# Kernel tuning notes

Measured on AMD Instinct MI355X. Metric: run time of the kernel, lower is better.

Reference implementation:

```python
import jax, jax.numpy as jnp
import numpy as np

NUM_HEADS = 4
EPS = 1e-5

def _proj(x, W, b):
    # 1x1x1 Conv3d == channel-wise linear: x [B,C,H,W,D], W [Cout,Cin], b [Cout]
    return jnp.einsum('oc,bchwd->bohwd', W, x) + b[None, :, None, None, None]

def setup_inputs() -> dict:
    key = jax.random.key(0)
    ks = jax.random.split(key, 12)
    B, C, H, W, D = 2, 128, 16, 16, 16
    s = 1.0 / np.sqrt(C)
    inp = {
        'query_features': jax.random.normal(ks[0], (B, C, H, W, D), jnp.float32),
        'key_value_features': jax.random.normal(ks[1], (B, C, H, W, D), jnp.float32),
        'Wq': jax.random.normal(ks[2], (C, C), jnp.float32) * s,
        'bq': jax.random.normal(ks[3], (C,), jnp.float32) * 0.01,
        'Wk': jax.random.normal(ks[4], (C, C), jnp.float32) * s,
        'bk': jax.random.normal(ks[5], (C,), jnp.float32) * 0.01,
        'Wv': jax.random.normal(ks[6], (C, C), jnp.float32) * s,
        'bv': jax.random.normal(ks[7], (C,), jnp.float32) * 0.01,
        'Wo': jax.random.normal(ks[8], (C, C), jnp.float32) * s,
        'bo': jax.random.normal(ks[9], (C,), jnp.float32) * 0.01,
    }
    return inp

def reference(query_features, key_value_features, Wq, bq, Wk, bk, Wv, bv, Wo, bo):
    B, C, H, W, D = query_features.shape
    hd = C // NUM_HEADS  # head_dim
    N = H * W * D
    Q = _proj(query_features, Wq, bq).reshape(B, NUM_HEADS, hd, N)
    K = _proj(key_value_features, Wk, bk).reshape(B, NUM_HEADS, hd, N)
    V = _proj(key_value_features, Wv, bv).reshape(B, NUM_HEADS, hd, N)
    scale = hd ** -0.5
    attn = jnp.einsum('bhdn,bhdm->bhnm', Q, K) * scale  # [B,h,N,N]
    attn = jax.nn.softmax(attn, axis=-1)
    out = jnp.einsum('bhnm,bhdm->bhdn', attn, V).reshape(B, C, H, W, D)
    out = _proj(out, Wo, bo)
    res = query_features + out
    # InstanceNorm3d (affine=False): normalize over spatial dims per (B,C)
    mu = jnp.mean(res, axis=(2, 3, 4), keepdims=True)
    var = jnp.var(res, axis=(2, 3, 4), keepdims=True)
    return (res - mu) * jax.lax.rsqrt(var + EPS)
```

## Files before the change

### kernel.cpp

```cpp
#include <hip/hip_runtime.h>
#include <hip/hip_bf16.h>

typedef unsigned short u16;
typedef unsigned int u32;
typedef __bf16 bf16_t;
typedef bf16_t bf16x8 __attribute__((ext_vector_type(8)));
typedef float f32x4 __attribute__((ext_vector_type(4)));

#define NTOT 4096
#define CCH 128

__device__ __forceinline__ float bf2f(u16 x) {
    return __uint_as_float(((u32)x) << 16);
}
__device__ __forceinline__ u32 pkbf(float a, float b) {
    __hip_bfloat162 h = __float22bfloat162_rn(make_float2(a, b));
    u32 r; __builtin_memcpy(&r, &h, 4); return r;
}
__device__ __forceinline__ u16 f2bf(float a) {
    return (u16)(pkbf(a, a) & 0xffffu);
}
union U4B8 { uint4 u4; u32 u[4]; bf16x8 v; };

__global__ __launch_bounds__(256) void proj_kernel(
    const float* __restrict__ xq, const float* __restrict__ xkv,
    const float* __restrict__ Wq, const float* __restrict__ bq_,
    const float* __restrict__ Wk, const float* __restrict__ bk_,
    const float* __restrict__ Wv, const float* __restrict__ bv_,
    u16* __restrict__ Qt, u16* __restrict__ Kt, u16* __restrict__ Vn)
{
    const int nt = blockIdx.x;
    const int ct = blockIdx.y;
    const int pb = blockIdx.z;
    const int p = pb >> 1, b = pb & 1;
    const float* X    = (p == 0) ? xq : xkv;
    const float* W    = (p == 0) ? Wq : (p == 1) ? Wk : Wv;
    const float* bias = (p == 0) ? bq_ : (p == 1) ? bk_ : bv_;
    const int n0 = nt * 64;
    const int tid = threadIdx.x;

    __shared__ u16 Xt[64 * 128];
    #pragma unroll
    for (int k = 0; k < 4; ++k) {
        int n = tid & 63;
        int c = (tid >> 6) + k * 4;
        float f[8];
        #pragma unroll
        for (int j = 0; j < 8; ++j)
            f[j] = X[((size_t)(b * CCH) + 8 * c + j) * NTOT + n0 + n];
        uint4 vv = {pkbf(f[0], f[1]), pkbf(f[2], f[3]), pkbf(f[4], f[5]), pkbf(f[6], f[7])};
        *(uint4*)(Xt + n * 128 + ((c ^ (n & 7)) * 8)) = vv;
    }
    __syncthreads();

    const int wave = tid >> 6, lane = tid & 63;
    const int quad = lane >> 4, l16 = lane & 15;
    f32x4 acc[2] = {{0.f, 0.f, 0.f, 0.f}, {0.f, 0.f, 0.f, 0.f}};

    #pragma unroll
    for (int kk = 0; kk < 4; ++kk) {
        bf16x8 bx = *(const bf16x8*)(Xt + (wave * 16 + l16) * 128 +
                                     (((kk * 4 + quad) ^ (l16 & 7)) * 8));
        #pragma unroll
        for (int hf = 0; hf < 2; ++hf) {
            const float* wrow = W + (size_t)(ct * 32 + hf * 16 + l16) * 128 + kk * 32 + quad * 8;
            float4 f0 = *(const float4*)(wrow);
            float4 f1 = *(const float4*)(wrow + 4);
            U4B8 aw;
            aw.u[0] = pkbf(f0.x, f0.y); aw.u[1] = pkbf(f0.z, f0.w);
            aw.u[2] = pkbf(f1.x, f1.y); aw.u[3] = pkbf(f1.z, f1.w);
            acc[hf] = __builtin_amdgcn_mfma_f32_16x16x32_bf16(aw.v, bx, acc[hf], 0, 0, 0);
        }
    }

    const float scl = (p == 0) ? 0.25503486703f : 1.0f;
    const int n = n0 + wave * 16 + l16;
    #pragma unroll
    for (int hf = 0; hf < 2; ++hf) {
        float4 b4 = *(const float4*)(bias + ct * 32 + hf * 16 + quad * 4);
        float v0 = (acc[hf][0] + b4.x) * scl;
        float v1 = (acc[hf][1] + b4.y) * scl;
        float v2 = (acc[hf][2] + b4.z) * scl;
        float v3 = (acc[hf][3] + b4.w) * scl;
        if (p < 2) {
            u16* dst = (p == 0 ? Qt : Kt) +
                ((size_t)(b * 4 + ct) * NTOT + n) * 32 + hf * 16 + quad * 4;
            uint2 vv = {pkbf(v0, v1), pkbf(v2, v3)};
            *(uint2*)dst = vv;
        } else {
            int c = ct * 32 + hf * 16 + quad * 4;
            u16* dst = Vn + (size_t)(b * CCH + c) * NTOT + n;
            dst[0 * NTOT] = f2bf(v0); dst[1 * NTOT] = f2bf(v1);
            dst[2 * NTOT] = f2bf(v2); dst[3 * NTOT] = f2bf(v3);
        }
    }
}

__global__ __launch_bounds__(256, 4) void flash_attn_kernel(
    const u16* __restrict__ Qt, const u16* __restrict__ Kt,
    const u16* __restrict__ Vn, u16* __restrict__ pO, float* __restrict__ pL)
{
    const int bh = blockIdx.z, kc = blockIdx.y;
    const int wave = threadIdx.x >> 6, lane = threadIdx.x & 63;
    const int q = lane >> 4, l16 = lane & 15;
    const int q0w = blockIdx.x * 128 + wave * 32;

    const u16* Qbh = Qt + (size_t)bh * NTOT * 32;
    const u16* Kbh = Kt + (size_t)bh * NTOT * 32;
    const u16* Vg  = Vn + ((size_t)((bh >> 2) * CCH + (bh & 3) * 32)) * NTOT;

    __shared__ u16 Kb[2][2048];
    __shared__ u16 Vb[2][2048];
    __shared__ u16 Pb[4][2048];

    const int kbase = kc * 1024;

    bf16x8 bq0 = *(const bf16x8*)(Qbh + (size_t)(q0w + l16) * 32 + q * 8);
    bf16x8 bq1 = *(const bf16x8*)(Qbh + (size_t)(q0w + 16 + l16) * 32 + q * 8);

    const size_t ksrc = (size_t)(wave * 16 + l16) * 32 + q * 8;
    const size_t vsrc = (size_t)((wave & 1) * 16 + l16) * NTOT + (wave >> 1) * 32 + q * 8;
    const int kv_dst = wave * 512 + lane * 8;

    uint4 kreg = *(const uint4*)(Kbh + (size_t)kbase * 32 + ksrc);
    uint4 vreg = *(const uint4*)(Vg + vsrc + kbase);
    *(uint4*)(&Kb[0][kv_dst]) = kreg;
    *(uint4*)(&Vb[0][kv_dst]) = vreg;
    __syncthreads();

    f32x4 o00 = {0,0,0,0}, o01 = {0,0,0,0};
    f32x4 o10 = {0,0,0,0}, o11 = {0,0,0,0};
    const f32x4 zero = {0,0,0,0};
    float lp0 = 0.f, lp1 = 0.f;

    u16* pw = &Pb[wave][0];
    const int pwr = (q >> 1) * 128 + l16 * 8 + (q & 1) * 4;

    for (int it = 0; it < 16; ++it) {
        const int cur = it & 1;
        if (it < 15) {
            const int m1 = kbase + (it + 1) * 64;
            kreg = *(const uint4*)(Kbh + (size_t)m1 * 32 + ksrc);
            vreg = *(const uint4*)(Vg + vsrc + m1);
        }
        f32x4 s0[4], s1[4];
        #pragma unroll
        for (int t = 0; t < 4; ++t) {
            bf16x8 ak = *(const bf16x8*)(&Kb[cur][t * 512 + lane * 8]);
            s0[t] = __builtin_amdgcn_mfma_f32_16x16x32_bf16(ak, bq0, zero, 0, 0, 0);
            s1[t] = __builtin_amdgcn_mfma_f32_16x16x32_bf16(ak, bq1, zero, 0, 0, 0);
        }
        #pragma unroll
        for (int t = 0; t < 4; ++t) {
            float p0 = __builtin_amdgcn_exp2f(s0[t][0]);
            float p1 = __builtin_amdgcn_exp2f(s0[t][1]);
            float p2 = __builtin_amdgcn_exp2f(s0[t][2]);
            float p3 = __builtin_amdgcn_exp2f(s0[t][3]);
            lp0 += (p0 + p1) + (p2 + p3);
            uint2 wv = {pkbf(p0, p1), pkbf(p2, p3)};
            *(uint2*)(pw + (t >> 1) * 512 + (t & 1) * 256 + pwr) = wv;
        }
        #pragma unroll
        for (int t = 0; t < 4; ++t) {
            float p0 = __builtin_amdgcn_exp2f(s1[t][0]);
            float p1 = __builtin_amdgcn_exp2f(s1[t][1]);
            float p2 = __builtin_amdgcn_exp2f(s1[t][2]);
            float p3 = __builtin_amdgcn_exp2f(s1[t][3]);
            lp1 += (p0 + p1) + (p2 + p3);
            uint2 wv = {pkbf(p0, p1), pkbf(p2, p3)};
            *(uint2*)(pw + 1024 + (t >> 1) * 512 + (t & 1) * 256 + pwr) = wv;
        }
        #pragma unroll
        for (int mc = 0; mc < 2; ++mc) {
            bf16x8 av0 = *(const bf16x8*)(&Vb[cur][(mc * 2 + 0) * 512 + lane * 8]);
            bf16x8 av1 = *(const bf16x8*)(&Vb[cur][(mc * 2 + 1) * 512 + lane * 8]);
            bf16x8 pb0 = *(const bf16x8*)(pw + mc * 512 + lane * 8);
            bf16x8 pb1 = *(const bf16x8*)(pw + 1024 + mc * 512 + lane * 8);
            o00 = __builtin_amdgcn_mfma_f32_16x16x32_bf16(av0, pb0, o00, 0, 0, 0);
            o01 = __builtin_amdgcn_mfma_f32_16x16x32_bf16(av1, pb0, o01, 0, 0, 0);
            o10 = __builtin_amdgcn_mfma_f32_16x16x32_bf16(av0, pb1, o10, 0, 0, 0);
            o11 = __builtin_amdgcn_mfma_f32_16x16x32_bf16(av1, pb1, o11, 0, 0, 0);
        }
        if (it < 15) {
            const int nb = (it + 1) & 1;
            *(uint4*)(&Kb[nb][kv_dst]) = kreg;
            *(uint4*)(&Vb[nb][kv_dst]) = vreg;
        }
        __syncthreads();
    }

    lp0 += __shfl_xor(lp0, 16); lp0 += __shfl_xor(lp0, 32);
    lp1 += __shfl_xor(lp1, 16); lp1 += __shfl_xor(lp1, 32);

    const size_t ob = ((size_t)(kc * 8 + bh) * NTOT + q0w + l16) * 32 + q * 4;
    uint2 w00 = {pkbf(o00[0], o00[1]), pkbf(o00[2], o00[3])};
    uint2 w01 = {pkbf(o01[0], o01[1]), pkbf(o01[2], o01[3])};
    uint2 w10 = {pkbf(o10[0], o10[1]), pkbf(o10[2], o10[3])};
    uint2 w11 = {pkbf(o11[0], o11[1]), pkbf(o11[2], o11[3])};
    *(uint2*)(pO + ob)            = w00;
    *(uint2*)(pO + ob + 16)       = w01;
    *(uint2*)(pO + ob + 512)      = w10;
    *(uint2*)(pO + ob + 512 + 16) = w11;
    if (q == 0) {
        pL[(size_t)(kc * 8 + bh) * NTOT + q0w + l16]      = lp0;
        pL[(size_t)(kc * 8 + bh) * NTOT + q0w + 16 + l16] = lp1;
    }
}

__global__ __launch_bounds__(256) void combine_kernel(
    const u16* __restrict__ pO, const float* __restrict__ pL,
    u16* __restrict__ attnT)
{
    const int idx = blockIdx.x * 256 + threadIdx.x;
    const int o  = idx & 3;
    const int n  = (idx >> 2) & 4095;
    const int bh = idx >> 14;
    float l = 0.f;
    #pragma unroll
    for (int kc = 0; kc < 4; ++kc)
        l += pL[(size_t)(kc * 8 + bh) * NTOT + n];
    float v[8];
    #pragma unroll
    for (int j = 0; j < 8; ++j) v[j] = 0.f;
    #pragma unroll
    for (int kc = 0; kc < 4; ++kc) {
        const u16* src = pO + ((size_t)(kc * 8 + bh) * NTOT + n) * 32 + o * 8;
        uint4 u = *(const uint4*)src;
        const u32 uu[4] = {u.x, u.y, u.z, u.w};
        #pragma unroll
        for (int j = 0; j < 4; ++j) {
            v[2 * j]     += bf2f((u16)(uu[j] & 0xffffu));
            v[2 * j + 1] += bf2f((u16)(uu[j] >> 16));
        }
    }
    const float inv = 1.0f / l;
    uint4 out = {pkbf(v[0] * inv, v[1] * inv), pkbf(v[2] * inv, v[3] * inv),
                 pkbf(v[4] * inv, v[5] * inv), pkbf(v[6] * inv, v[7] * inv)};
    const int b = bh >> 2, h = bh & 3;
    *(uint4*)(attnT + ((size_t)(b * NTOT) + n) * 128 + h * 32 + o * 8) = out;
}

__global__ __launch_bounds__(256) void outproj_kernel(
    const float* __restrict__ xq, const u16* __restrict__ attnT,
    const float* __restrict__ Wo, const float* __restrict__ bo,
    float* __restrict__ res, float* __restrict__ partS, float* __restrict__ partQ)
{
    const int nt = blockIdx.x, ct = blockIdx.y, b = blockIdx.z;
    const int n0 = nt * 64;
    const int tid = threadIdx.x;

    __shared__ u16 Xt[64 * 128];
    #pragma unroll
    for (int k = 0; k < 4; ++k) {
        int cid = tid + k * 256;
        int n = cid >> 4;
        int ch = cid & 15;
        uint4 u = *(const uint4*)(attnT + ((size_t)(b * NTOT) + n0 + n) * 128 + ch * 8);
        *(uint4*)(Xt + n * 128 + ((ch ^ (n & 7)) * 8)) = u;
    }
    __syncthreads();

    const int wave = tid >> 6, lane = tid & 63;
    const int quad = lane >> 4, l16 = lane & 15;
    f32x4 acc = {0.f, 0.f, 0.f, 0.f};
    #pragma unroll
    for (int kk = 0; kk < 4; ++kk) {
        bf16x8 bx = *(const bf16x8*)(Xt + (wave * 16 + l16) * 128 +
                                     (((kk * 4 + quad) ^ (l16 & 7)) * 8));
        const float* wrow = Wo + (size_t)(ct * 16 + l16) * 128 + kk * 32 + quad * 8;
        float4 f0 = *(const float4*)(wrow);
        float4 f1 = *(const float4*)(wrow + 4);
        U4B8 aw;
        aw.u[0] = pkbf(f0.x, f0.y); aw.u[1] = pkbf(f0.z, f0.w);
        aw.u[2] = pkbf(f1.x, f1.y); aw.u[3] = pkbf(f1.z, f1.w);
        acc = __builtin_amdgcn_mfma_f32_16x16x32_bf16(aw.v, bx, acc, 0, 0, 0);
    }

    const int n = n0 + wave * 16 + l16;
    float4 b4 = *(const float4*)(bo + ct * 16 + quad * 4);
    const float bb[4] = {b4.x, b4.y, b4.z, b4.w};
    float sv[4], qv[4];
    #pragma unroll
    for (int r = 0; r < 4; ++r) {
        int c = ct * 16 + quad * 4 + r;
        float v = acc[r] + bb[r] + xq[(size_t)(b * CCH + c) * NTOT + n];
        res[(size_t)(b * CCH + c) * NTOT + n] = v;
        sv[r] = v;
        qv[r] = v * v;
    }
    #pragma unroll
    for (int off = 1; off < 16; off <<= 1) {
        #pragma unroll
        for (int r = 0; r < 4; ++r) {
            sv[r] += __shfl_xor(sv[r], off);
            qv[r] += __shfl_xor(qv[r], off);
        }
    }
    if (l16 == 0) {
        int tile = nt * 4 + wave;
        #pragma unroll
        for (int r = 0; r < 4; ++r) {
            int c = ct * 16 + quad * 4 + r;
            partS[(size_t)(b * CCH + c) * 256 + tile] = sv[r];
            partQ[(size_t)(b * CCH + c) * 256 + tile] = qv[r];
        }
    }
}

__global__ __launch_bounds__(256) void norm_kernel(
    const float* __restrict__ res, const float* __restrict__ partS,
    const float* __restrict__ partQ, float* __restrict__ out)
{
    const int c = blockIdx.x, b = blockIdx.y;
    const int tid = threadIdx.x;
    const size_t row = (size_t)(b * CCH + c);
    __shared__ float rs[4], rq[4];
    float s = partS[row * 256 + tid];
    float q = partQ[row * 256 + tid];
    #pragma unroll
    for (int off = 1; off < 64; off <<= 1) {
        s += __shfl_xor(s, off);
        q += __shfl_xor(q, off);
    }
    const int wv = tid >> 6, ln = tid & 63;
    if (ln == 0) { rs[wv] = s; rq[wv] = q; }
    __syncthreads();
    float ts = rs[0] + rs[1] + rs[2] + rs[3];
    float tq = rq[0] + rq[1] + rq[2] + rq[3];
    float mu  = ts * (1.0f / 4096.0f);
    float var = tq * (1.0f / 4096.0f) - mu * mu;
    float inv = rsqrtf(var + 1e-5f);
    const size_t base = row * NTOT;
    #pragma unroll
    for (int j = 0; j < 4; ++j) {
        int n = tid * 4 + j * 1024;
        float4 v = *(const float4*)(res + base + n);
        float4 o;
        o.x = (v.x - mu) * inv; o.y = (v.y - mu) * inv;
        o.z = (v.z - mu) * inv; o.w = (v.w - mu) * inv;
        *(float4*)(out + base + n) = o;
    }
}

extern "C" void kernel_launch(void* const* d_in, const int* in_sizes, int n_in,
                              void* d_out, int out_size, void* d_ws, size_t ws_size,
                              hipStream_t stream)
{
    const float* xq  = (const float*)d_in[0];
    const float* xkv = (const float*)d_in[1];
    const float* Wq  = (const float*)d_in[2];
    const float* bq  = (const float*)d_in[3];
    const float* Wk  = (const float*)d_in[4];
    const float* bk  = (const float*)d_in[5];
    const float* Wv  = (const float*)d_in[6];
    const float* bv  = (const float*)d_in[7];
    const float* Wo  = (const float*)d_in[8];
    const float* bo  = (const float*)d_in[9];
    float* out = (float*)d_out;

    char* ws = (char*)d_ws;
    const size_t MB = (size_t)1 << 20;
    u16* Qt = (u16*)(ws + 0 * MB);
    u16* Kt = (u16*)(ws + 2 * MB);
    u16* Vn = (u16*)(ws + 4 * MB);
    u16*   pO = (u16*)(ws + 6 * MB);
    float* pL = (float*)d_out;
    u16* attnT = (u16*)(ws + 0 * MB);
    float* res   = (float*)(ws + 2 * MB);
    float* partS = (float*)(ws + 6 * MB);
    float* partQ = (float*)(ws + 6 * MB + 262144);

    proj_kernel<<<dim3(64, 4, 6), 256, 0, stream>>>(xq, xkv, Wq, bq, Wk, bk, Wv, bv, Qt, Kt, Vn);
    flash_attn_kernel<<<dim3(32, 4, 8), 256, 0, stream>>>(Qt, Kt, Vn, pO, pL);
    combine_kernel<<<dim3(512), 256, 0, stream>>>(pO, pL, attnT);
    outproj_kernel<<<dim3(64, 8, 2), 256, 0, stream>>>(xq, attnT, Wo, bo, res, partS, partQ);
    norm_kernel<<<dim3(128, 2), 256, 0, stream>>>(res, partS, partQ, out);
}
```

Measured before the change: 137.0 us.

## Pre-convert weights, widen projection tiles, enlarge attention tiles, fuse combine into outproj

Adds a prep kernel that converts all weight matrices to bf16 once and folds the Q scale into Wq and bq. Projection blocks now compute all 128 output channels from LDS-staged weights instead of reloading fp32 weights per 32-channel tile. The attention kernel processes 64 queries per wave, reusing each K/V tile across more MFMAs, and lowers its occupancy hint. The separate combine kernel is removed and its split-K reduction is fused into the output projection, which now computes 64 channels per block. This cuts redundant X reloads and one launch, at the cost of higher register and LDS pressure and fewer blocks.

```diff
diff --git a/kernel.cpp b/kernel.cpp
--- a/kernel.cpp
+++ b/kernel.cpp
@@ -9,6 +9,7 @@
 
 #define NTOT 4096
 #define CCH 128
+#define QSCL 0.25503486703f
 
 __device__ __forceinline__ float bf2f(u16 x) {
     return __uint_as_float(((u32)x) << 16);
@@ -20,26 +21,43 @@
 __device__ __forceinline__ u16 f2bf(float a) {
     return (u16)(pkbf(a, a) & 0xffffu);
 }
-union U4B8 { uint4 u4; u32 u[4]; bf16x8 v; };
-
-__global__ __launch_bounds__(256) void proj_kernel(
+
+__global__ __launch_bounds__(256) void prep_kernel(
+    const float* __restrict__ Wq, const float* __restrict__ Wk,
+    const float* __restrict__ Wv, const float* __restrict__ Wo,
+    const float* __restrict__ bq,
+    u16* __restrict__ Wqb, u16* __restrict__ Wkb,
+    u16* __restrict__ Wvb, u16* __restrict__ Wob,
+    float* __restrict__ bqs)
+{
+    const int idx = blockIdx.x * 256 + threadIdx.x;
+    const int m = idx >> 13;
+    const int e = idx & 8191;
+    const float* src = (m == 0) ? Wq : (m == 1) ? Wk : (m == 2) ? Wv : Wo;
+    u32* dst = (u32*)((m == 0) ? Wqb : (m == 1) ? Wkb : (m == 2) ? Wvb : Wob);
+    const float s = (m == 0) ? QSCL : 1.0f;
+    float2 f = ((const float2*)src)[e];
+    dst[e] = pkbf(f.x * s, f.y * s);
+    if (idx < CCH) bqs[idx] = bq[idx] * QSCL;
+}
+
+__global__ __launch_bounds__(256, 4) void proj_kernel(
     const float* __restrict__ xq, const float* __restrict__ xkv,
-    const float* __restrict__ Wq, const float* __restrict__ bq_,
-    const float* __restrict__ Wk, const float* __restrict__ bk_,
-    const float* __restrict__ Wv, const float* __restrict__ bv_,
+    const u16* __restrict__ Wqb, const float* __restrict__ bqs,
+    const u16* __restrict__ Wkb, const float* __restrict__ bk_,
+    const u16* __restrict__ Wvb, const float* __restrict__ bv_,
     u16* __restrict__ Qt, u16* __restrict__ Kt, u16* __restrict__ Vn)
 {
-    const int nt = blockIdx.x;
-    const int ct = blockIdx.y;
-    const int pb = blockIdx.z;
-    const int p = pb >> 1, b = pb & 1;
+    const int nt = blockIdx.x, p = blockIdx.y, b = blockIdx.z;
     const float* X    = (p == 0) ? xq : xkv;
-    const float* W    = (p == 0) ? Wq : (p == 1) ? Wk : Wv;
-    const float* bias = (p == 0) ? bq_ : (p == 1) ? bk_ : bv_;
+    const u16*   Wb   = (p == 0) ? Wqb : (p == 1) ? Wkb : Wvb;
+    const float* bias = (p == 0) ? bqs : (p == 1) ? bk_ : bv_;
     const int n0 = nt * 64;
     const int tid = threadIdx.x;
 
     __shared__ u16 Xt[64 * 128];
+    __shared__ u16 Wl[128 * 136];
+
     #pragma unroll
     for (int k = 0; k < 4; ++k) {
         int n = tid & 63;
@@ -51,44 +69,48 @@
         uint4 vv = {pkbf(f[0], f[1]), pkbf(f[2], f[3]), pkbf(f[4], f[5]), pkbf(f[6], f[7])};
         *(uint4*)(Xt + n * 128 + ((c ^ (n & 7)) * 8)) = vv;
     }
+    #pragma unroll
+    for (int k = 0; k < 8; ++k) {
+        int id = tid + k * 256;
+        int row = id >> 4;
+        int off = (id & 15) * 8;
+        *(uint4*)(Wl + row * 136 + off) = *(const uint4*)(Wb + row * 128 + off);
+    }
     __syncthreads();
 
     const int wave = tid >> 6, lane = tid & 63;
     const int quad = lane >> 4, l16 = lane & 15;
-    f32x4 acc[2] = {{0.f, 0.f, 0.f, 0.f}, {0.f, 0.f, 0.f, 0.f}};
+    f32x4 acc[8];
+    #pragma unroll
+    for (int cf = 0; cf < 8; ++cf) acc[cf] = (f32x4){0.f, 0.f, 0.f, 0.f};
 
     #pragma unroll
     for (int kk = 0; kk < 4; ++kk) {
         bf16x8 bx = *(const bf16x8*)(Xt + (wave * 16 + l16) * 128 +
                                      (((kk * 4 + quad) ^ (l16 & 7)) * 8));
         #pragma unroll
-        for (int hf = 0; hf < 2; ++hf) {
-            const float* wrow = W + (size_t)(ct * 32 + hf * 16 + l16) * 128 + kk * 32 + quad * 8;
-            float4 f0 = *(const float4*)(wrow);
-            float4 f1 = *(const float4*)(wrow + 4);
-            U4B8 aw;
-            aw.u[0] = pkbf(f0.x, f0.y); aw.u[1] = pkbf(f0.z, f0.w);
-            aw.u[2] = pkbf(f1.x, f1.y); aw.u[3] = pkbf(f1.z, f1.w);
-            acc[hf] = __builtin_amdgcn_mfma_f32_16x16x32_bf16(aw.v, bx, acc[hf], 0, 0, 0);
-        }
-    }
-
-    const float scl = (p == 0) ? 0.25503486703f : 1.0f;
+        for (int cf = 0; cf < 8; ++cf) {
+            bf16x8 aw = *(const bf16x8*)(Wl + (cf * 16 + l16) * 136 + kk * 32 + quad * 8);
+            acc[cf] = __builtin_amdgcn_mfma_f32_16x16x32_bf16(aw, bx, acc[cf], 0, 0, 0);
+        }
+    }
+
     const int n = n0 + wave * 16 + l16;
     #pragma unroll
-    for (int hf = 0; hf < 2; ++hf) {
-        float4 b4 = *(const float4*)(bias + ct * 32 + hf * 16 + quad * 4);
-        float v0 = (acc[hf][0] + b4.x) * scl;
-        float v1 = (acc[hf][1] + b4.y) * scl;
-        float v2 = (acc[hf][2] + b4.z) * scl;
-        float v3 = (acc[hf][3] + b4.w) * scl;
+    for (int cf = 0; cf < 8; ++cf) {
+        float4 b4 = *(const float4*)(bias + cf * 16 + quad * 4);
+        float v0 = acc[cf][0] + b4.x;
+        float v1 = acc[cf][1] + b4.y;
+        float v2 = acc[cf][2] + b4.z;
+        float v3 = acc[cf][3] + b4.w;
         if (p < 2) {
-            u16* dst = (p == 0 ? Qt : Kt) +
-                ((size_t)(b * 4 + ct) * NTOT + n) * 32 + hf * 16 + quad * 4;
+            const int h = cf >> 1;
+            const int d0 = (cf & 1) * 16 + quad * 4;
+            u16* dst = (p == 0 ? Qt : Kt) + ((size_t)(b * 4 + h) * NTOT + n) * 32 + d0;
             uint2 vv = {pkbf(v0, v1), pkbf(v2, v3)};
             *(uint2*)dst = vv;
         } else {
-            int c = ct * 32 + hf * 16 + quad * 4;
+            int c = cf * 16 + quad * 4;
             u16* dst = Vn + (size_t)(b * CCH + c) * NTOT + n;
             dst[0 * NTOT] = f2bf(v0); dst[1 * NTOT] = f2bf(v1);
             dst[2 * NTOT] = f2bf(v2); dst[3 * NTOT] = f2bf(v3);
@@ -96,14 +118,14 @@
     }
 }
 
-__global__ __launch_bounds__(256, 4) void flash_attn_kernel(
+__global__ __launch_bounds__(256, 2) void flash_attn_kernel(
     const u16* __restrict__ Qt, const u16* __restrict__ Kt,
     const u16* __restrict__ Vn, u16* __restrict__ pO, float* __restrict__ pL)
 {
     const int bh = blockIdx.z, kc = blockIdx.y;
     const int wave = threadIdx.x >> 6, lane = threadIdx.x & 63;
     const int q = lane >> 4, l16 = lane & 15;
-    const int q0w = blockIdx.x * 128 + wave * 32;
+    const int q0w = blockIdx.x * 256 + wave * 64;
 
     const u16* Qbh = Qt + (size_t)bh * NTOT * 32;
     const u16* Kbh = Kt + (size_t)bh * NTOT * 32;
@@ -111,12 +133,14 @@
 
     __shared__ u16 Kb[2][2048];
     __shared__ u16 Vb[2][2048];
-    __shared__ u16 Pb[4][2048];
+    __shared__ u16 Pb[4][1024];
 
     const int kbase = kc * 1024;
 
-    bf16x8 bq0 = *(const bf16x8*)(Qbh + (size_t)(q0w + l16) * 32 + q * 8);
-    bf16x8 bq1 = *(const bf16x8*)(Qbh + (size_t)(q0w + 16 + l16) * 32 + q * 8);
+    bf16x8 bq[4];
+    #pragma unroll
+    for (int g = 0; g < 4; ++g)
+        bq[g] = *(const bf16x8*)(Qbh + (size_t)(q0w + g * 16 + l16) * 32 + q * 8);
 
     const size_t ksrc = (size_t)(wave * 16 + l16) * 32 + q * 8;
     const size_t vsrc = (size_t)((wave & 1) * 16 + l16) * NTOT + (wave >> 1) * 32 + q * 8;
@@ -128,13 +152,19 @@
     *(uint4*)(&Vb[0][kv_dst]) = vreg;
     __syncthreads();
 
-    f32x4 o00 = {0,0,0,0}, o01 = {0,0,0,0};
-    f32x4 o10 = {0,0,0,0}, o11 = {0,0,0,0};
+    f32x4 o[4][2];
+    #pragma unroll
+    for (int g = 0; g < 4; ++g) {
+        o[g][0] = (f32x4){0,0,0,0};
+        o[g][1] = (f32x4){0,0,0,0};
+    }
     const f32x4 zero = {0,0,0,0};
-    float lp0 = 0.f, lp1 = 0.f;
+    float lp[4] = {0.f, 0.f, 0.f, 0.f};
 
     u16* pw = &Pb[wave][0];
     const int pwr = (q >> 1) * 128 + l16 * 8 + (q & 1) * 4;
+    const int prd0 = 0 * 512 + lane * 8;
+    const int prd1 = 1 * 512 + lane * 8;
 
     for (int it = 0; it < 16; ++it) {
         const int cur = it & 1;
@@ -143,43 +173,36 @@
             kreg = *(const uint4*)(Kbh + (size_t)m1 * 32 + ksrc);
             vreg = *(const uint4*)(Vg + vsrc + m1);
         }
-        f32x4 s0[4], s1[4];
+        f32x4 s[4][4];
         #pragma unroll
         for (int t = 0; t < 4; ++t) {
             bf16x8 ak = *(const bf16x8*)(&Kb[cur][t * 512 + lane * 8]);
-            s0[t] = __builtin_amdgcn_mfma_f32_16x16x32_bf16(ak, bq0, zero, 0, 0, 0);
-            s1[t] = __builtin_amdgcn_mfma_f32_16x16x32_bf16(ak, bq1, zero, 0, 0, 0);
-        }
-        #pragma unroll
-        for (int t = 0; t < 4; ++t) {
-            float p0 = __builtin_amdgcn_exp2f(s0[t][0]);
-            float p1 = __builtin_amdgcn_exp2f(s0[t][1]);
-            float p2 = __builtin_amdgcn_exp2f(s0[t][2]);
-            float p3 = __builtin_amdgcn_exp2f(s0[t][3]);
-            lp0 += (p0 + p1) + (p2 + p3);
-            uint2 wv = {pkbf(p0, p1), pkbf(p2, p3)};
-            *(uint2*)(pw + (t >> 1) * 512 + (t & 1) * 256 + pwr) = wv;
-        }
-        #pragma unroll
-        for (int t = 0; t < 4; ++t) {
-            float p0 = __builtin_amdgcn_exp2f(s1[t][0]);
-            float p1 = __builtin_amdgcn_exp2f(s1[t][1]);
-            float p2 = __builtin_amdgcn_exp2f(s1[t][2]);
-            float p3 = __builtin_amdgcn_exp2f(s1[t][3]);
-            lp1 += (p0 + p1) + (p2 + p3);
-            uint2 wv = {pkbf(p0, p1), pkbf(p2, p3)};
-            *(uint2*)(pw + 1024 + (t >> 1) * 512 + (t & 1) * 256 + pwr) = wv;
-        }
-        #pragma unroll
-        for (int mc = 0; mc < 2; ++mc) {
-            bf16x8 av0 = *(const bf16x8*)(&Vb[cur][(mc * 2 + 0) * 512 + lane * 8]);
-            bf16x8 av1 = *(const bf16x8*)(&Vb[cur][(mc * 2 + 1) * 512 + lane * 8]);
-            bf16x8 pb0 = *(const bf16x8*)(pw + mc * 512 + lane * 8);
-            bf16x8 pb1 = *(const bf16x8*)(pw + 1024 + mc * 512 + lane * 8);
-            o00 = __builtin_amdgcn_mfma_f32_16x16x32_bf16(av0, pb0, o00, 0, 0, 0);
-            o01 = __builtin_amdgcn_mfma_f32_16x16x32_bf16(av1, pb0, o01, 0, 0, 0);
-            o10 = __builtin_amdgcn_mfma_f32_16x16x32_bf16(av0, pb1, o10, 0, 0, 0);
-            o11 = __builtin_amdgcn_mfma_f32_16x16x32_bf16(av1, pb1, o11, 0, 0, 0);
+            #pragma unroll
+            for (int g = 0; g < 4; ++g)
+                s[g][t] = __builtin_amdgcn_mfma_f32_16x16x32_bf16(ak, bq[g], zero, 0, 0, 0);
+        }
+        bf16x8 av00 = *(const bf16x8*)(&Vb[cur][0 * 512 + lane * 8]);
+        bf16x8 av01 = *(const bf16x8*)(&Vb[cur][1 * 512 + lane * 8]);
+        bf16x8 av10 = *(const bf16x8*)(&Vb[cur][2 * 512 + lane * 8]);
+        bf16x8 av11 = *(const bf16x8*)(&Vb[cur][3 * 512 + lane * 8]);
+        #pragma unroll
+        for (int g = 0; g < 4; ++g) {
+            #pragma unroll
+            for (int t = 0; t < 4; ++t) {
+                float p0 = __builtin_amdgcn_exp2f(s[g][t][0]);
+                float p1 = __builtin_amdgcn_exp2f(s[g][t][1]);
+                float p2 = __builtin_amdgcn_exp2f(s[g][t][2]);
+                float p3 = __builtin_amdgcn_exp2f(s[g][t][3]);
+                lp[g] += (p0 + p1) + (p2 + p3);
+                uint2 wv = {pkbf(p0, p1), pkbf(p2, p3)};
+                *(uint2*)(pw + (t >> 1) * 512 + (t & 1) * 256 + pwr) = wv;
+            }
+            bf16x8 pb0 = *(const bf16x8*)(pw + prd0);
+            bf16x8 pb1 = *(const bf16x8*)(pw + prd1);
+            o[g][0] = __builtin_amdgcn_mfma_f32_16x16x32_bf16(av00, pb0, o[g][0], 0, 0, 0);
+            o[g][1] = __builtin_amdgcn_mfma_f32_16x16x32_bf16(av01, pb0, o[g][1], 0, 0, 0);
+            o[g][0] = __builtin_amdgcn_mfma_f32_16x16x32_bf16(av10, pb1, o[g][0], 0, 0, 0);
+            o[g][1] = __builtin_amdgcn_mfma_f32_16x16x32_bf16(av11, pb1, o[g][1], 0, 0, 0);
         }
         if (it < 15) {
             const int nb = (it + 1) & 1;
@@ -189,60 +212,24 @@
         __syncthreads();
     }
 
-    lp0 += __shfl_xor(lp0, 16); lp0 += __shfl_xor(lp0, 32);
-    lp1 += __shfl_xor(lp1, 16); lp1 += __shfl_xor(lp1, 32);
-
-    const size_t ob = ((size_t)(kc * 8 + bh) * NTOT + q0w + l16) * 32 + q * 4;
-    uint2 w00 = {pkbf(o00[0], o00[1]), pkbf(o00[2], o00[3])};
-    uint2 w01 = {pkbf(o01[0], o01[1]), pkbf(o01[2], o01[3])};
-    uint2 w10 = {pkbf(o10[0], o10[1]), pkbf(o10[2], o10[3])};
-    uint2 w11 = {pkbf(o11[0], o11[1]), pkbf(o11[2], o11[3])};
-    *(uint2*)(pO + ob)            = w00;
-    *(uint2*)(pO + ob + 16)       = w01;
-    *(uint2*)(pO + ob + 512)      = w10;
-    *(uint2*)(pO + ob + 512 + 16) = w11;
-    if (q == 0) {
-        pL[(size_t)(kc * 8 + bh) * NTOT + q0w + l16]      = lp0;
-        pL[(size_t)(kc * 8 + bh) * NTOT + q0w + 16 + l16] = lp1;
-    }
-}
-
-__global__ __launch_bounds__(256) void combine_kernel(
+    #pragma unroll
+    for (int g = 0; g < 4; ++g) {
+        lp[g] += __shfl_xor(lp[g], 16);
+        lp[g] += __shfl_xor(lp[g], 32);
+        const size_t ob = ((size_t)(kc * 8 + bh) * NTOT + q0w + g * 16 + l16) * 32 + q * 4;
+        uint2 w0 = {pkbf(o[g][0][0], o[g][0][1]), pkbf(o[g][0][2], o[g][0][3])};
+        uint2 w1 = {pkbf(o[g][1][0], o[g][1][1]), pkbf(o[g][1][2], o[g][1][3])};
+        *(uint2*)(pO + ob)      = w0;
+        *(uint2*)(pO + ob + 16) = w1;
+        if (q == 0)
+            pL[(size_t)(kc * 8 + bh) * NTOT + q0w + g * 16 + l16] = lp[g];
+    }
+}
+
+__global__ __launch_bounds__(256, 4) void outproj_kernel(
+    const float* __restrict__ xq,
     const u16* __restrict__ pO, const float* __restrict__ pL,
-    u16* __restrict__ attnT)
-{
-    const int idx = blockIdx.x * 256 + threadIdx.x;
-    const int o  = idx & 3;
-    const int n  = (idx >> 2) & 4095;
-    const int bh = idx >> 14;
-    float l = 0.f;
-    #pragma unroll
-    for (int kc = 0; kc < 4; ++kc)
-        l += pL[(size_t)(kc * 8 + bh) * NTOT + n];
-    float v[8];
-    #pragma unroll
-    for (int j = 0; j < 8; ++j) v[j] = 0.f;
-    #pragma unroll
-    for (int kc = 0; kc < 4; ++kc) {
-        const u16* src = pO + ((size_t)(kc * 8 + bh) * NTOT + n) * 32 + o * 8;
-        uint4 u = *(const uint4*)src;
-        const u32 uu[4] = {u.x, u.y, u.z, u.w};
-        #pragma unroll
-        for (int j = 0; j < 4; ++j) {
-            v[2 * j]     += bf2f((u16)(uu[j] & 0xffffu));
-            v[2 * j + 1] += bf2f((u16)(uu[j] >> 16));
-        }
-    }
-    const float inv = 1.0f / l;
-    uint4 out = {pkbf(v[0] * inv, v[1] * inv), pkbf(v[2] * inv, v[3] * inv),
-                 pkbf(v[4] * inv, v[5] * inv), pkbf(v[6] * inv, v[7] * inv)};
-    const int b = bh >> 2, h = bh & 3;
-    *(uint4*)(attnT + ((size_t)(b * NTOT) + n) * 128 + h * 32 + o * 8) = out;
-}
-
-__global__ __launch_bounds__(256) void outproj_kernel(
-    const float* __restrict__ xq, const u16* __restrict__ attnT,
-    const float* __restrict__ Wo, const float* __restrict__ bo,
+    const u16* __restrict__ Wob, const float* __restrict__ bo,
     float* __restrict__ res, float* __restrict__ partS, float* __restrict__ partQ)
 {
     const int nt = blockIdx.x, ct = blockIdx.y, b = blockIdx.z;
@@ -250,59 +237,93 @@
     const int tid = threadIdx.x;
 
     __shared__ u16 Xt[64 * 128];
+    __shared__ u16 Wl[64 * 136];
+
     #pragma unroll
     for (int k = 0; k < 4; ++k) {
         int cid = tid + k * 256;
         int n = cid >> 4;
         int ch = cid & 15;
-        uint4 u = *(const uint4*)(attnT + ((size_t)(b * NTOT) + n0 + n) * 128 + ch * 8);
-        *(uint4*)(Xt + n * 128 + ((ch ^ (n & 7)) * 8)) = u;
+        int bh = b * 4 + (ch >> 2);
+        int d0 = (ch & 3) * 8;
+        float l = 0.f;
+        float v[8];
+        #pragma unroll
+        for (int j = 0; j < 8; ++j) v[j] = 0.f;
+        #pragma unroll
+        for (int kcc = 0; kcc < 4; ++kcc) {
+            const size_t nrow = (size_t)(kcc * 8 + bh) * NTOT + n0 + n;
+            l += pL[nrow];
+            uint4 u = *(const uint4*)(pO + nrow * 32 + d0);
+            const u32 uu[4] = {u.x, u.y, u.z, u.w};
+            #pragma unroll
+            for (int j = 0; j < 4; ++j) {
+                v[2 * j]     += bf2f((u16)(uu[j] & 0xffffu));
+                v[2 * j + 1] += bf2f((u16)(uu[j] >> 16));
+            }
+        }
+        const float inv = 1.0f / l;
+        uint4 vv = {pkbf(v[0] * inv, v[1] * inv), pkbf(v[2] * inv, v[3] * inv),
+                    pkbf(v[4] * inv, v[5] * inv), pkbf(v[6] * inv, v[7] * inv)};
+        *(uint4*)(Xt + n * 128 + ((ch ^ (n & 7)) * 8)) = vv;
+    }
+    #pragma unroll
+    for (int k = 0; k < 4; ++k) {
+        int id = tid + k * 256;
+        int row = id >> 4;
+        int off = (id & 15) * 8;
+        *(uint4*)(Wl + row * 136 + off) =
+            *(const uint4*)(Wob + (size_t)(ct * 64 + row) * 128 + off);
     }
     __syncthreads();
 
     const int wave = tid >> 6, lane = tid & 63;
     const int quad = lane >> 4, l16 = lane & 15;
-    f32x4 acc = {0.f, 0.f, 0.f, 0.f};
+    f32x4 acc[4];
+    #pragma unroll
+    for (int cf = 0; cf < 4; ++cf) acc[cf] = (f32x4){0.f, 0.f, 0.f, 0.f};
+
     #pragma unroll
     for (int kk = 0; kk < 4; ++kk) {
         bf16x8 bx = *(const bf16x8*)(Xt + (wave * 16 + l16) * 128 +
                                      (((kk * 4 + quad) ^ (l16 & 7)) * 8));
-        const float* wrow = Wo + (size_t)(ct * 16 + l16) * 128 + kk * 32 + quad * 8;
-        float4 f0 = *(const float4*)(wrow);
-        float4 f1 = *(const float4*)(wrow + 4);
-        U4B8 aw;
-        aw.u[0] = pkbf(f0.x, f0.y); aw.u[1] = pkbf(f0.z, f0.w);
-        aw.u[2] = pkbf(f1.x, f1.y); aw.u[3] = pkbf(f1.z, f1.w);
-        acc = __builtin_amdgcn_mfma_f32_16x16x32_bf16(aw.v, bx, acc, 0, 0, 0);
+        #pragma unroll
+        for (int cf = 0; cf < 4; ++cf) {
+            bf16x8 aw = *(const bf16x8*)(Wl + (cf * 16 + l16) * 136 + kk * 32 + quad * 8);
+            acc[cf] = __builtin_amdgcn_mfma_f32_16x16x32_bf16(aw, bx, acc[cf], 0, 0, 0);
+        }
     }
 
     const int n = n0 + wave * 16 + l16;
-    float4 b4 = *(const float4*)(bo + ct * 16 + quad * 4);
-    const float bb[4] = {b4.x, b4.y, b4.z, b4.w};
-    float sv[4], qv[4];
-    #pragma unroll
-    for (int r = 0; r < 4; ++r) {
-        int c = ct * 16 + quad * 4 + r;
-        float v = acc[r] + bb[r] + xq[(size_t)(b * CCH + c) * NTOT + n];
-        res[(size_t)(b * CCH + c) * NTOT + n] = v;
-        sv[r] = v;
-        qv[r] = v * v;
-    }
-    #pragma unroll
-    for (int off = 1; off < 16; off <<= 1) {
+    const int tile = nt * 4 + wave;
+    #pragma unroll
+    for (int cf = 0; cf < 4; ++cf) {
+        float4 b4 = *(const float4*)(bo + ct * 64 + cf * 16 + quad * 4);
+        const float bb[4] = {b4.x, b4.y, b4.z, b4.w};
+        float sv[4], qv[4];
         #pragma unroll
         for (int r = 0; r < 4; ++r) {
-            sv[r] += __shfl_xor(sv[r], off);
-            qv[r] += __shfl_xor(qv[r], off);
-        }
-    }
-    if (l16 == 0) {
-        int tile = nt * 4 + wave;
-        #pragma unroll
-        for (int r = 0; r < 4; ++r) {
-            int c = ct * 16 + quad * 4 + r;
-            partS[(size_t)(b * CCH + c) * 256 + tile] = sv[r];
-            partQ[(size_t)(b * CCH + c) * 256 + tile] = qv[r];
+            int c = ct * 64 + cf * 16 + quad * 4 + r;
+            float v = acc[cf][r] + bb[r] + xq[(size_t)(b * CCH + c) * NTOT + n];
+            res[(size_t)(b * CCH + c) * NTOT + n] = v;
+            sv[r] = v;
+            qv[r] = v * v;
+        }
+        #pragma unroll
+        for (int off = 1; off < 16; off <<= 1) {
+            #pragma unroll
+            for (int r = 0; r < 4; ++r) {
+                sv[r] += __shfl_xor(sv[r], off);
+                qv[r] += __shfl_xor(qv[r], off);
+            }
+        }
+        if (l16 == 0) {
+            #pragma unroll
+            for (int r = 0; r < 4; ++r) {
+                int c = ct * 64 + cf * 16 + quad * 4 + r;
+                partS[(size_t)(b * CCH + c) * 256 + tile] = sv[r];
+                partQ[(size_t)(b * CCH + c) * 256 + tile] = qv[r];
+            }
         }
     }
 }
@@ -363,16 +384,20 @@
     u16* Qt = (u16*)(ws + 0 * MB);
     u16* Kt = (u16*)(ws + 2 * MB);
     u16* Vn = (u16*)(ws + 4 * MB);
-    u16*   pO = (u16*)(ws + 6 * MB);
-    float* pL = (float*)d_out;
-    u16* attnT = (u16*)(ws + 0 * MB);
-    float* res   = (float*)(ws + 2 * MB);
-    float* partS = (float*)(ws + 6 * MB);
-    float* partQ = (float*)(ws + 6 * MB + 262144);
-
-    proj_kernel<<<dim3(64, 4, 6), 256, 0, stream>>>(xq, xkv, Wq, bq, Wk, bk, Wv, bv, Qt, Kt, Vn);
-    flash_attn_kernel<<<dim3(32, 4, 8), 256, 0, stream>>>(Qt, Kt, Vn, pO, pL);
-    combine_kernel<<<dim3(512), 256, 0, stream>>>(pO, pL, attnT);
-    outproj_kernel<<<dim3(64, 8, 2), 256, 0, stream>>>(xq, attnT, Wo, bo, res, partS, partQ);
+    u16* pO = (u16*)(ws + 6 * MB);
+    float* pL = (float*)(ws + 14 * MB);
+    u16* Wqb = (u16*)(ws + 15 * MB);
+    u16* Wkb = Wqb + 16384;
+    u16* Wvb = Wkb + 16384;
+    u16* Wob = Wvb + 16384;
+    float* bqs = (float*)(Wob + 16384);
+    float* res   = (float*)(ws + 16 * MB);
+    float* partS = (float*)(ws + 20 * MB);
+    float* partQ = (float*)(ws + 20 * MB + 262144);
+
+    prep_kernel<<<dim3(128), 256, 0, stream>>>(Wq, Wk, Wv, Wo, bq, Wqb, Wkb, Wvb, Wob, bqs);
+    proj_kernel<<<dim3(64, 3, 2), 256, 0, stream>>>(xq, xkv, Wqb, bqs, Wkb, bk, Wvb, bv, Qt, Kt, Vn);
+    flash_attn_kernel<<<dim3(16, 4, 8), 256, 0, stream>>>(Qt, Kt, Vn, pO, pL);
+    outproj_kernel<<<dim3(64, 2, 2), 256, 0, stream>>>(xq, pO, pL, Wob, bo, res, partS, partQ);
     norm_kernel<<<dim3(128, 2), 256, 0, stream>>>(res, partS, partQ, out);
 }
```

After: 126.7 us. 7.5% less time.
